# Kernel tuning notes

Hardware: AMD Instinct MI355X
Metric: run time of the kernel (lower is better)

The kernel has to match this reference:

```python
import jax, jax.numpy as jnp
import numpy as np

N, E = 50000, 800000          # nodes, directed edges
F_IN = 80                     # 16 unique sensors * 5 features
H, C = 4, 96                  # num_heads, hidden_dim
D = H * C                     # 384 = concat output dim per GAT layer
NC = 20                       # n_classes = number of components
NEG_SLOPE = 0.2               # PyG GATv2Conv default negative_slope
EPS = 1e-5                    # LayerNorm eps


def layer_norm(x, g, b):
    mu = x.mean(-1, keepdims=True)
    var = x.var(-1, keepdims=True)
    return (x - mu) * jax.lax.rsqrt(var + EPS) * g + b


def gatv2(x, src, dst, Wsrc, Wdst, att, bias):
    # GATv2Conv (concat=True): e_ij = att . leaky_relu(Wsrc x_j + Wdst x_i),
    # alpha = segment-softmax over dst, out_i = sum_j alpha_ij * (Wsrc x_j)
    n = x.shape[0]
    xs = (x @ Wsrc).reshape(n, H, C)
    xd = (x @ Wdst).reshape(n, H, C)
    m = jax.nn.leaky_relu(xs[src] + xd[dst], NEG_SLOPE)      # [E,H,C]
    e = jnp.einsum('ehc,hc->eh', m, att)                     # [E,H]
    emax = jax.ops.segment_max(e, dst, num_segments=n)       # [N,H]
    ex = jnp.exp(e - emax[dst])
    denom = jax.ops.segment_sum(ex, dst, num_segments=n)
    alpha = ex / (denom[dst] + 1e-16)                        # [E,H]
    out = jax.ops.segment_sum(alpha[:, :, None] * xs[src], dst, num_segments=n)
    return out.reshape(n, D) + bias


def setup_inputs():
    key = jax.random.key(0)
    ks = jax.random.split(key, 16)

    def w(k, shape, fan):
        return (jax.random.normal(k, shape, jnp.float32) / np.float32(np.sqrt(fan)))

    inp = {
        'x': jax.random.normal(ks[0], (N, F_IN), jnp.float32),
        'edge_index': jax.random.randint(ks[1], (2, E), 0, N, jnp.int32),
    }
    dims = [F_IN, D, D]
    i = 2
    for l in range(3):
        inp[f'Wsrc{l}'] = w(ks[i], (dims[l], D), dims[l]); i += 1
        inp[f'Wdst{l}'] = w(ks[i], (dims[l], D), dims[l]); i += 1
        inp[f'att{l}'] = w(ks[i], (H, C), C); i += 1
        inp[f'b{l}'] = jnp.zeros((D,), jnp.float32)
        inp[f'g{l}'] = jnp.ones((D,), jnp.float32)
        inp[f'be{l}'] = jnp.zeros((D,), jnp.float32)
    inp['Wc1'] = w(ks[i], (D, C), D); i += 1
    inp['bc1'] = jnp.zeros((C,), jnp.float32)
    inp['gc'] = jnp.ones((C,), jnp.float32)
    inp['bec'] = jnp.zeros((C,), jnp.float32)
    inp['Wc2'] = w(ks[i], (C, NC), C)
    inp['bc2'] = jnp.zeros((NC,), jnp.float32)
    return inp


def reference(x, edge_index,
              Wsrc0, Wdst0, att0, b0, g0, be0,
              Wsrc1, Wdst1, att1, b1, g1, be1,
              Wsrc2, Wdst2, att2, b2, g2, be2,
              Wc1, bc1, gc, bec, Wc2, bc2):
    src, dst = edge_index[0], edge_index[1]
    layers = [(Wsrc0, Wdst0, att0, b0, g0, be0),
              (Wsrc1, Wdst1, att1, b1, g1, be1),
              (Wsrc2, Wdst2, att2, b2, g2, be2)]
    h = x
    for (Ws, Wd, a, b, g, be) in layers:
        h = gatv2(h, src, dst, Ws, Wd, a, b)
        h = jax.nn.elu(layer_norm(h, g, be))   # dropout: identity in eval mode
    h = jax.nn.relu(h @ Wc1 + bc1)
    h = layer_norm(h, gc, bec)
    return h @ Wc2 + bc2
```

## Files before the change

kernel.cpp:

```cpp
#include <hip/hip_runtime.h>
#include <math.h>

#define D 384
#define NCLS 20
#define FIN 80
#define CH 96

typedef unsigned int u32t;
typedef unsigned short u16t;
typedef __attribute__((ext_vector_type(8))) short bf16x8;
typedef __attribute__((ext_vector_type(4))) float f32x4;

__device__ __forceinline__ u16t f2bf(float f) {
    u32t b = __float_as_uint(f);
    u32t r = (b + 0x7FFFu + ((b >> 16) & 1u)) >> 16;
    return (u16t)r;
}
__device__ __forceinline__ float bfl(u32t u) { return __uint_as_float(u << 16); }
__device__ __forceinline__ float bfh(u32t u) { return __uint_as_float(u & 0xFFFF0000u); }

#define GLOAD16(g, l)                                                            \
    __builtin_amdgcn_global_load_lds(                                            \
        (const __attribute__((address_space(1))) void*)(g),                      \
        (__attribute__((address_space(3))) void*)(l), 16, 0, 0)


__global__ void k_zero(int* p, int n) {
    int i = blockIdx.x * blockDim.x + threadIdx.x;
    if (i < n) p[i] = 0;
}

__global__ void k_hist(const int* __restrict__ dst, int* __restrict__ deg, int E) {
    int i = blockIdx.x * blockDim.x + threadIdx.x;
    if (i < E) atomicAdd(&deg[dst[i]], 1);
}

__global__ __launch_bounds__(256) void k_scan1(const int* __restrict__ deg,
                                               int* __restrict__ offs,
                                               int* __restrict__ bsum, int n) {
    __shared__ int sh[256];
    int t = threadIdx.x, i = blockIdx.x * 256 + t;
    int v = (i < n) ? deg[i] : 0;
    sh[t] = v;
    __syncthreads();
    for (int o = 1; o < 256; o <<= 1) {
        int a = (t >= o) ? sh[t - o] : 0;
        __syncthreads();
        sh[t] += a;
        __syncthreads();
    }
    if (i < n) offs[i] = sh[t] - v;
    if (t == 255) bsum[blockIdx.x] = sh[255];
}

__global__ __launch_bounds__(256) void k_scan2(int* __restrict__ bsum, int nb,
                                               int* __restrict__ offs, int n) {
    __shared__ int sh[256];
    int t = threadIdx.x;
    int v = (t < nb) ? bsum[t] : 0;
    sh[t] = v;
    __syncthreads();
    for (int o = 1; o < 256; o <<= 1) {
        int a = (t >= o) ? sh[t - o] : 0;
        __syncthreads();
        sh[t] += a;
        __syncthreads();
    }
    if (t < nb) bsum[t] = sh[t] - v;
    if (t == 255) offs[n] = sh[255];
}

__global__ __launch_bounds__(256) void k_scan3(int* __restrict__ offs,
                                               int* __restrict__ cursor,
                                               const int* __restrict__ bsum, int n) {
    int i = blockIdx.x * 256 + threadIdx.x;
    if (i < n) {
        int o = offs[i] + bsum[blockIdx.x];
        offs[i] = o;
        cursor[i] = o;
    }
}

__global__ void k_scatter(const int* __restrict__ src, const int* __restrict__ dst,
                          int* __restrict__ cursor, int* __restrict__ csr_srcb, int E) {
    int i = blockIdx.x * blockDim.x + threadIdx.x;
    if (i < E) {
        int p = atomicAdd(&cursor[dst[i]], 1);
        csr_srcb[p] = src[i] * 384;
    }
}


__global__ __launch_bounds__(256) void k_cvt_all(
    const float* __restrict__ x,
    const float* __restrict__ Ws0, const float* __restrict__ Wd0,
    const float* __restrict__ Ws1, const float* __restrict__ Wd1,
    const float* __restrict__ Ws2, const float* __restrict__ Wd2,
    const float* __restrict__ Wc1,
    u16t* __restrict__ xbf,
    u16t* __restrict__ WT0s, u16t* __restrict__ WT0d,
    u16t* __restrict__ WT1s, u16t* __restrict__ WT1d,
    u16t* __restrict__ WT2s, u16t* __restrict__ WT2d,
    u16t* __restrict__ Wc1T, int N) {
    const int s96 = 384 * 96, s384 = 384 * 384, sc1 = 128 * 384;
    int i = blockIdx.x * 256 + threadIdx.x;

    int n0 = N * 96;
    if (i < n0) {
        int r = i / 96, c = i - r * 96;
        xbf[i] = f2bf(c < FIN ? x[r * FIN + c] : 0.f);
        return;
    }
    i -= n0;
    if (i < 2 * s96) {
        const float* W = (i < s96) ? Ws0 : Wd0;
        u16t* O = (i < s96) ? WT0s : WT0d;
        int k2 = (i < s96) ? i : i - s96;
        int c = k2 / 96, k = k2 - c * 96;
        O[k2] = f2bf(k < FIN ? W[(size_t)k * D + c] : 0.f);
        return;
    }
    i -= 2 * s96;
    if (i < 4 * s384) {
        int w = i / s384, k2 = i - w * s384;
        const float* W = (w == 0) ? Ws1 : (w == 1) ? Wd1 : (w == 2) ? Ws2 : Wd2;
        u16t* O = (w == 0) ? WT1s : (w == 1) ? WT1d : (w == 2) ? WT2s : WT2d;
        int c = k2 / 384, k = k2 - c * 384;
        O[k2] = f2bf(W[(size_t)k * D + c]);
        return;
    }
    i -= 4 * s384;
    if (i < sc1) {
        int c = i / D, k = i - c * D;
        Wc1T[i] = f2bf(c < CH ? Wc1[(size_t)k * CH + c] : 0.f);
    }
}


__global__ __launch_bounds__(256) void k_mm(const u16t* __restrict__ A,
                                            const u16t* __restrict__ BT,
                                            u16t* __restrict__ C, int Kp, int ostride) {
    __shared__ u16t Al[4][128][8];
    __shared__ u16t Bl[4][128][8];
    const int t = threadIdx.x;
    const int wave = t >> 6, lane = t & 63;
    const int wr = wave >> 1, wc = wave & 1;
    const int bm0 = blockIdx.x * 128;
    const int bn0 = blockIdx.y * 128;
    const int col16 = lane & 15, kc = lane >> 4;

    f32x4 acc[4][4] = {};

    const u16t* asrc0 = A + (size_t)(bm0 + lane) * Kp + wave * 8;
    const u16t* asrc1 = A + (size_t)(bm0 + 64 + lane) * Kp + wave * 8;
    const u16t* bsrc0 = BT + (size_t)(bn0 + lane) * Kp + wave * 8;
    const u16t* bsrc1 = BT + (size_t)(bn0 + 64 + lane) * Kp + wave * 8;
    u16t* alds0 = &Al[wave][0][0];
    u16t* alds1 = &Al[wave][64][0];
    u16t* blds0 = &Bl[wave][0][0];
    u16t* blds1 = &Bl[wave][64][0];

    for (int k0 = 0; k0 < Kp; k0 += 32) {
        GLOAD16(asrc0 + k0, alds0);
        GLOAD16(asrc1 + k0, alds1);
        GLOAD16(bsrc0 + k0, blds0);
        GLOAD16(bsrc1 + k0, blds1);
        __syncthreads();

        bf16x8 a[4], b[4];
#pragma unroll
        for (int m = 0; m < 4; m++)
            a[m] = *(const bf16x8*)&Al[kc][wr * 64 + m * 16 + col16][0];
#pragma unroll
        for (int n = 0; n < 4; n++)
            b[n] = *(const bf16x8*)&Bl[kc][wc * 64 + n * 16 + col16][0];
#pragma unroll
        for (int m = 0; m < 4; m++)
#pragma unroll
            for (int n = 0; n < 4; n++)
                acc[m][n] = __builtin_amdgcn_mfma_f32_16x16x32_bf16(
                    a[m], b[n], acc[m][n], 0, 0, 0);
        __syncthreads();
    }

#pragma unroll
    for (int m = 0; m < 4; m++) {
#pragma unroll
        for (int n = 0; n < 4; n++) {
#pragma unroll
            for (int j = 0; j < 4; j++) {
                int row = bm0 + wr * 64 + m * 16 + (lane >> 4) * 4 + j;
                int col = bn0 + wc * 64 + n * 16 + col16;
                C[(size_t)row * ostride + col] = f2bf(acc[m][n][j]);
            }
        }
    }
}


__global__ __launch_bounds__(256) void k_mmh(const u16t* __restrict__ A,
                                             const u16t* __restrict__ BT,
                                             const float* __restrict__ bc1,
                                             float* __restrict__ Yh) {
    __shared__ u16t Al[4][128][8];
    __shared__ u16t Bl[4][128][8];
    const int t = threadIdx.x;
    const int wave = t >> 6, lane = t & 63;
    const int wr = wave >> 1, wc = wave & 1;
    const int bm0 = blockIdx.x * 128;
    const int col16 = lane & 15, kc = lane >> 4;

    f32x4 acc[4][4] = {};

    const u16t* asrc0 = A + (size_t)(bm0 + lane) * D + wave * 8;
    const u16t* asrc1 = A + (size_t)(bm0 + 64 + lane) * D + wave * 8;
    const u16t* bsrc0 = BT + (size_t)lane * D + wave * 8;
    const u16t* bsrc1 = BT + (size_t)(64 + lane) * D + wave * 8;
    u16t* alds0 = &Al[wave][0][0];
    u16t* alds1 = &Al[wave][64][0];
    u16t* blds0 = &Bl[wave][0][0];
    u16t* blds1 = &Bl[wave][64][0];

    for (int k0 = 0; k0 < D; k0 += 32) {
        GLOAD16(asrc0 + k0, alds0);
        GLOAD16(asrc1 + k0, alds1);
        GLOAD16(bsrc0 + k0, blds0);
        GLOAD16(bsrc1 + k0, blds1);
        __syncthreads();

        bf16x8 a[4], b[4];
#pragma unroll
        for (int m = 0; m < 4; m++)
            a[m] = *(const bf16x8*)&Al[kc][wr * 64 + m * 16 + col16][0];
#pragma unroll
        for (int n = 0; n < 4; n++)
            b[n] = *(const bf16x8*)&Bl[kc][wc * 64 + n * 16 + col16][0];
#pragma unroll
        for (int m = 0; m < 4; m++)
#pragma unroll
            for (int n = 0; n < 4; n++)
                acc[m][n] = __builtin_amdgcn_mfma_f32_16x16x32_bf16(
                    a[m], b[n], acc[m][n], 0, 0, 0);
        __syncthreads();
    }

#pragma unroll
    for (int m = 0; m < 4; m++) {
#pragma unroll
        for (int n = 0; n < 4; n++) {
            int col = wc * 64 + n * 16 + col16;
            if (col < CH) {
                float bc = bc1[col];
#pragma unroll
                for (int j = 0; j < 4; j++) {
                    int row = bm0 + wr * 64 + m * 16 + (lane >> 4) * 4 + j;
                    Yh[(size_t)row * CH + col] = fmaxf(acc[m][n][j] + bc, 0.f);
                }
            }
        }
    }
}


__global__ __launch_bounds__(256) void k_gat(const u32t* __restrict__ XSXD,
                                             const float* __restrict__ att,
                                             const float* __restrict__ bias,
                                             const float* __restrict__ gamma,
                                             const float* __restrict__ beta,
                                             const int* __restrict__ offs,
                                             const int* __restrict__ csr_srcb,
                                             u16t* __restrict__ Hout,
                                             int N) {
    int wave = threadIdx.x >> 6;
    int lane = threadIdx.x & 63;
    int node = blockIdx.x * 4 + wave;
    if (node >= N) return;
    int c0 = lane * 6;
    int lo3 = lane * 3;

    const u32t* xdp = XSXD + (size_t)node * 384 + 192 + lo3;
    u32t d0 = xdp[0], d1 = xdp[1], d2 = xdp[2];
    float xd[6] = {bfl(d0), bfh(d0), bfl(d1), bfh(d1), bfl(d2), bfh(d2)};
    float attr[6];
#pragma unroll
    for (int k = 0; k < 6; k++) attr[k] = att[c0 + k] * 1.44269504f;

    float m = -INFINITY, denom = 0.f;
    float acc[6] = {0.f, 0.f, 0.f, 0.f, 0.f, 0.f};
    int e0 = offs[node], e1 = offs[node + 1];

    for (int base = e0; base < e1; base += 64) {
        int cnt = min(64, e1 - base);
        u32t midx = (lane < cnt) ? (u32t)csr_srcb[base + lane] : 0u;
        u32t off = __builtin_amdgcn_readlane(midx, 0);
        const u32t* p = XSXD + off + lo3;
        u32t a0 = p[0], a1 = p[1], a2 = p[2];

        for (int j = 0; j < cnt; j++) {
            u32t b0 = a0, b1 = a1, b2 = a2;
            if (j + 1 < cnt) {
                u32t offn = __builtin_amdgcn_readlane(midx, j + 1);
                const u32t* pn = XSXD + offn + lo3;
                a0 = pn[0]; a1 = pn[1]; a2 = pn[2];
            }
            float xs[6] = {bfl(b0), bfh(b0), bfl(b1), bfh(b1), bfl(b2), bfh(b2)};
            float part = 0.f;
#pragma unroll
            for (int k = 0; k < 6; k++) {
                float v = xs[k] + xd[k];
                part = fmaf(fmaxf(v, 0.2f * v), attr[k], part);
            }
#pragma unroll
            for (int o = 1; o < 16; o <<= 1) part += __shfl_xor(part, o, 64);

            if (__builtin_expect(__any(part - m > 8.0f), 0)) {
                float nm = fmaxf(m, part);
                float r = __builtin_amdgcn_exp2f(m - nm);
                float pp = __builtin_amdgcn_exp2f(part - nm);
                denom = denom * r + pp;
#pragma unroll
                for (int k = 0; k < 6; k++) acc[k] = fmaf(pp, xs[k], acc[k] * r);
                m = nm;
            } else {
                float pp = __builtin_amdgcn_exp2f(part - m);
                denom += pp;
#pragma unroll
                for (int k = 0; k < 6; k++) acc[k] = fmaf(pp, xs[k], acc[k]);
            }
        }
    }

    float inv = 1.f / (denom + 1e-16f);
    float v[6];
    float s1 = 0.f;
#pragma unroll
    for (int k = 0; k < 6; k++) { v[k] = acc[k] * inv + bias[c0 + k]; s1 += v[k]; }
#pragma unroll
    for (int o = 1; o < 64; o <<= 1) s1 += __shfl_xor(s1, o, 64);
    float mu = s1 * (1.f / 384.f);
    float s2 = 0.f;
#pragma unroll
    for (int k = 0; k < 6; k++) { float d = v[k] - mu; s2 += d * d; }
#pragma unroll
    for (int o = 1; o < 64; o <<= 1) s2 += __shfl_xor(s2, o, 64);
    float rstd = rsqrtf(s2 * (1.f / 384.f) + 1e-5f);

    float ov[6];
#pragma unroll
    for (int k = 0; k < 6; k++) {
        float y = (v[k] - mu) * rstd * gamma[c0 + k] + beta[c0 + k];
        ov[k] = y > 0.f ? y : __expf(y) - 1.f;
    }
    u32t w0 = (u32t)f2bf(ov[0]) | ((u32t)f2bf(ov[1]) << 16);
    u32t w1 = (u32t)f2bf(ov[2]) | ((u32t)f2bf(ov[3]) << 16);
    u32t w2 = (u32t)f2bf(ov[4]) | ((u32t)f2bf(ov[5]) << 16);
    u32t* hp = (u32t*)Hout + (size_t)node * 192 + lo3;
    hp[0] = w0; hp[1] = w1; hp[2] = w2;
}


__global__ __launch_bounds__(256) void k_lnout(const float* __restrict__ Yh,
                                               const float* __restrict__ gc,
                                               const float* __restrict__ bec,
                                               const float* __restrict__ Wc2,
                                               const float* __restrict__ bc2,
                                               float* __restrict__ out, int N) {
    __shared__ float w2[CH * NCLS];
    __shared__ float ln[8][CH];
    int t = threadIdx.x;
    int g = t >> 5, tl = t & 31;
    int node = blockIdx.x * 8 + g;

    for (int i = t; i < CH * NCLS; i += 256) w2[i] = Wc2[i];

    if (node < N) {
        const float* yp = Yh + (size_t)node * CH;
        float y0 = yp[tl], y1 = yp[32 + tl], y2 = yp[64 + tl];
        float s = y0 + y1 + y2;
#pragma unroll
        for (int o = 1; o < 32; o <<= 1) s += __shfl_xor(s, o, 32);
        float mu = s * (1.f / CH);
        float d0 = y0 - mu, d1 = y1 - mu, d2 = y2 - mu;
        float q = d0 * d0 + d1 * d1 + d2 * d2;
#pragma unroll
        for (int o = 1; o < 32; o <<= 1) q += __shfl_xor(q, o, 32);
        float rstd = rsqrtf(q * (1.f / CH) + 1e-5f);
        ln[g][tl]      = d0 * rstd * gc[tl]      + bec[tl];
        ln[g][32 + tl] = d1 * rstd * gc[32 + tl] + bec[32 + tl];
        ln[g][64 + tl] = d2 * rstd * gc[64 + tl] + bec[64 + tl];
    }
    __syncthreads();

    if (node < N && tl < NCLS) {
        float o = bc2[tl];
        for (int c = 0; c < CH; c++) o += ln[g][c] * w2[c * NCLS + tl];
        out[(size_t)node * NCLS + tl] = o;
    }
}


extern "C" void kernel_launch(void* const* d_in, const int* in_sizes, int n_in,
                              void* d_out, int out_size, void* d_ws, size_t ws_size,
                              hipStream_t stream) {
    const float* x        = (const float*)d_in[0];
    const int*   eidx     = (const int*)d_in[1];
    const float* Wsrc[3]  = {(const float*)d_in[2],  (const float*)d_in[8],  (const float*)d_in[14]};
    const float* Wdst[3]  = {(const float*)d_in[3],  (const float*)d_in[9],  (const float*)d_in[15]};
    const float* attw[3]  = {(const float*)d_in[4],  (const float*)d_in[10], (const float*)d_in[16]};
    const float* bia[3]   = {(const float*)d_in[5],  (const float*)d_in[11], (const float*)d_in[17]};
    const float* gam[3]   = {(const float*)d_in[6],  (const float*)d_in[12], (const float*)d_in[18]};
    const float* bet[3]   = {(const float*)d_in[7],  (const float*)d_in[13], (const float*)d_in[19]};
    const float* Wc1 = (const float*)d_in[20];
    const float* bc1 = (const float*)d_in[21];
    const float* gc  = (const float*)d_in[22];
    const float* bec = (const float*)d_in[23];
    const float* Wc2 = (const float*)d_in[24];
    const float* bc2 = (const float*)d_in[25];

    const int N = in_sizes[0] / FIN;
    const int E = in_sizes[1] / 2;
    const int Mpad = ((N + 127) / 128) * 128;
    const int* srcp = eidx;
    const int* dstp = eidx + E;

    u16t* xbf  = (u16t*)d_ws;
    u16t* XSXD = xbf + (size_t)Mpad * 96;
    u16t* Hbf  = XSXD + (size_t)Mpad * 768;
    u16t* WT0s = Hbf + (size_t)Mpad * D;
    u16t* WT0d = WT0s + 384 * 96;
    u16t* WT1s = WT0d + 384 * 96;
    u16t* WT1d = WT1s + 384 * 384;
    u16t* WT2s = WT1d + 384 * 384;
    u16t* WT2d = WT2s + 384 * 384;
    u16t* Wc1T = WT2d + 384 * 384;
    float* Yh  = (float*)(Wc1T + 128 * 384);
    int* offs    = (int*)(Yh + (size_t)Mpad * CH);
    int* cursor  = offs + (N + 1);
    int* deg     = cursor + (N + 1);
    int* bsum    = deg + N;
    int* csr_srcb = bsum + 512;

    const int nb = (N + 255) / 256;

    k_zero<<<nb, 256, 0, stream>>>(deg, N);
    k_hist<<<(E + 255) / 256, 256, 0, stream>>>(dstp, deg, E);
    k_scan1<<<nb, 256, 0, stream>>>(deg, offs, bsum, N);
    k_scan2<<<1, 256, 0, stream>>>(bsum, nb, offs, N);
    k_scan3<<<nb, 256, 0, stream>>>(offs, cursor, bsum, N);
    k_scatter<<<(E + 255) / 256, 256, 0, stream>>>(srcp, dstp, cursor, csr_srcb, E);

    {
        long total = (long)N * 96 + 2L * (384 * 96) + 4L * (384 * 384) + 128L * 384;
        int cblocks = (int)((total + 255) / 256);
        k_cvt_all<<<cblocks, 256, 0, stream>>>(
            x, Wsrc[0], Wdst[0], Wsrc[1], Wdst[1], Wsrc[2], Wdst[2], Wc1,
            xbf, WT0s, WT0d, WT1s, WT1d, WT2s, WT2d, Wc1T, N);
    }

    dim3 gmm(Mpad / 128, 768 / 128);
    int gatGrid = (N + 3) / 4;

    k_mm<<<gmm, 256, 0, stream>>>(xbf, WT0s, XSXD, 96, 768);
    k_gat<<<gatGrid, 256, 0, stream>>>((const u32t*)XSXD, attw[0], bia[0], gam[0], bet[0],
                                       offs, csr_srcb, Hbf, N);
    k_mm<<<gmm, 256, 0, stream>>>(Hbf, WT1s, XSXD, D, 768);
    k_gat<<<gatGrid, 256, 0, stream>>>((const u32t*)XSXD, attw[1], bia[1], gam[1], bet[1],
                                       offs, csr_srcb, Hbf, N);
    k_mm<<<gmm, 256, 0, stream>>>(Hbf, WT2s, XSXD, D, 768);
    k_gat<<<gatGrid, 256, 0, stream>>>((const u32t*)XSXD, attw[2], bia[2], gam[2], bet[2],
                                       offs, csr_srcb, Hbf, N);

    k_mmh<<<Mpad / 128, 256, 0, stream>>>(Hbf, Wc1T, bc1, Yh);
    k_lnout<<<(N + 7) / 8, 256, 0, stream>>>(Yh, gc, bec, Wc2, bc2,
                                             (float*)d_out, N);
}
```

Measured before the change: 749.8 us.

## Process two edges per iteration in GAT aggregation and swap GEMM grid order

The GAT edge loop now handles two neighbor edges per iteration. It prefetches two rows ahead and interleaves the two attention-logit reductions and online-softmax updates, which raises memory-level parallelism and ILP in the latency-bound gather. Separately, the GEMM grid is transposed so consecutive blocks share the same A row tile across the six N tiles, which should improve L2 reuse of the activation matrix. The cost is more registers per thread in the GAT kernel and a tail path for odd edge counts.

```diff
diff --git a/kernel.cpp b/kernel.cpp
--- a/kernel.cpp
+++ b/kernel.cpp
@@ -145,8 +145,8 @@
     const int t = threadIdx.x;
     const int wave = t >> 6, lane = t & 63;
     const int wr = wave >> 1, wc = wave & 1;
-    const int bm0 = blockIdx.x * 128;
-    const int bn0 = blockIdx.y * 128;
+    const int bm0 = blockIdx.y * 128;
+    const int bn0 = blockIdx.x * 128;
     const int col16 = lane & 15, kc = lane >> 4;
 
     f32x4 acc[4][4] = {};
@@ -292,18 +292,75 @@
     for (int base = e0; base < e1; base += 64) {
         int cnt = min(64, e1 - base);
         u32t midx = (lane < cnt) ? (u32t)csr_srcb[base + lane] : 0u;
-        u32t off = __builtin_amdgcn_readlane(midx, 0);
-        const u32t* p = XSXD + off + lo3;
-        u32t a0 = p[0], a1 = p[1], a2 = p[2];
-
-        for (int j = 0; j < cnt; j++) {
-            u32t b0 = a0, b1 = a1, b2 = a2;
-            if (j + 1 < cnt) {
-                u32t offn = __builtin_amdgcn_readlane(midx, j + 1);
+
+        u32t a00, a01, a02, a10 = 0, a11 = 0, a12 = 0;
+        {
+            u32t off0 = __builtin_amdgcn_readlane(midx, 0);
+            const u32t* p0 = XSXD + off0 + lo3;
+            a00 = p0[0]; a01 = p0[1]; a02 = p0[2];
+            if (cnt > 1) {
+                u32t off1 = __builtin_amdgcn_readlane(midx, 1);
+                const u32t* p1 = XSXD + off1 + lo3;
+                a10 = p1[0]; a11 = p1[1]; a12 = p1[2];
+            }
+        }
+
+        int j = 0;
+        for (; j + 1 < cnt; j += 2) {
+            u32t b00 = a00, b01 = a01, b02 = a02;
+            u32t b10 = a10, b11 = a11, b12 = a12;
+            if (j + 2 < cnt) {
+                u32t offn = __builtin_amdgcn_readlane(midx, j + 2);
                 const u32t* pn = XSXD + offn + lo3;
-                a0 = pn[0]; a1 = pn[1]; a2 = pn[2];
-            }
-            float xs[6] = {bfl(b0), bfh(b0), bfl(b1), bfh(b1), bfl(b2), bfh(b2)};
+                a00 = pn[0]; a01 = pn[1]; a02 = pn[2];
+            }
+            if (j + 3 < cnt) {
+                u32t offn = __builtin_amdgcn_readlane(midx, j + 3);
+                const u32t* pn = XSXD + offn + lo3;
+                a10 = pn[0]; a11 = pn[1]; a12 = pn[2];
+            }
+            float xs0[6] = {bfl(b00), bfh(b00), bfl(b01), bfh(b01), bfl(b02), bfh(b02)};
+            float xs1[6] = {bfl(b10), bfh(b10), bfl(b11), bfh(b11), bfl(b12), bfh(b12)};
+            float part0 = 0.f, part1 = 0.f;
+#pragma unroll
+            for (int k = 0; k < 6; k++) {
+                float v0 = xs0[k] + xd[k];
+                float v1 = xs1[k] + xd[k];
+                part0 = fmaf(fmaxf(v0, 0.2f * v0), attr[k], part0);
+                part1 = fmaf(fmaxf(v1, 0.2f * v1), attr[k], part1);
+            }
+#pragma unroll
+            for (int o = 1; o < 16; o <<= 1) {
+                part0 += __shfl_xor(part0, o, 64);
+                part1 += __shfl_xor(part1, o, 64);
+            }
+
+            if (__builtin_expect(__any(fmaxf(part0, part1) - m > 8.0f), 0)) {
+                float nm = fmaxf(m, part0);
+                float r = __builtin_amdgcn_exp2f(m - nm);
+                float pp = __builtin_amdgcn_exp2f(part0 - nm);
+                denom = denom * r + pp;
+#pragma unroll
+                for (int k = 0; k < 6; k++) acc[k] = fmaf(pp, xs0[k], acc[k] * r);
+                m = nm;
+                nm = fmaxf(m, part1);
+                r = __builtin_amdgcn_exp2f(m - nm);
+                pp = __builtin_amdgcn_exp2f(part1 - nm);
+                denom = denom * r + pp;
+#pragma unroll
+                for (int k = 0; k < 6; k++) acc[k] = fmaf(pp, xs1[k], acc[k] * r);
+                m = nm;
+            } else {
+                float pp0 = __builtin_amdgcn_exp2f(part0 - m);
+                float pp1 = __builtin_amdgcn_exp2f(part1 - m);
+                denom += pp0 + pp1;
+#pragma unroll
+                for (int k = 0; k < 6; k++)
+                    acc[k] = fmaf(pp1, xs1[k], fmaf(pp0, xs0[k], acc[k]));
+            }
+        }
+        if (j < cnt) {
+            float xs[6] = {bfl(a00), bfh(a00), bfl(a01), bfh(a01), bfl(a02), bfh(a02)};
             float part = 0.f;
 #pragma unroll
             for (int k = 0; k < 6; k++) {
@@ -457,7 +514,7 @@
             xbf, WT0s, WT0d, WT1s, WT1d, WT2s, WT2d, Wc1T, N);
     }
 
-    dim3 gmm(Mpad / 128, 768 / 128);
+    dim3 gmm(768 / 128, Mpad / 128);
     int gatGrid = (N + 3) / 4;
 
     k_mm<<<gmm, 256, 0, stream>>>(xbf, WT0s, XSXD, 96, 768);
```

Measured after the change: 760.0 us. No clear change (+1.4%).
